# Kernel optimization log

Measured on AMD Instinct MI355X. Metric: run time of the kernel, lower is better.

Reference implementation:

```python
import jax, jax.numpy as jnp
import numpy as np

EMB = 1024
HEADS = 16


def setup_inputs() -> dict:
    key = jax.random.key(0)
    ks = jax.random.split(key, 5)
    s = 1.0 / np.sqrt(EMB).astype(np.float32)
    return {
        "x": jax.random.normal(ks[0], (4, 2048, EMB), dtype=jnp.float32),
        "Wq": jax.random.normal(ks[1], (EMB, EMB), dtype=jnp.float32) * s,
        "bq": jnp.zeros((EMB,), dtype=jnp.float32),
        "Wk": jax.random.normal(ks[2], (EMB, EMB), dtype=jnp.float32) * s,
        "bk": jnp.zeros((EMB,), dtype=jnp.float32),
        "Wv": jax.random.normal(ks[3], (EMB, EMB), dtype=jnp.float32) * s,
        "bv": jnp.zeros((EMB,), dtype=jnp.float32),
        "Wo": jax.random.normal(ks[4], (EMB, EMB), dtype=jnp.float32) * s,
        "bo": jnp.zeros((EMB,), dtype=jnp.float32),
    }


def reference(x, Wq, bq, Wk, bk, Wv, bv, Wo, bo):
    b, n, e = x.shape
    h = HEADS
    d = e // h
    # QKV projections, split heads: [b, n, e] -> [b, h, n, d]
    def split_heads(t):
        return t.reshape(b, n, h, d).transpose(0, 2, 1, 3)
    q = split_heads(x @ Wq + bq)
    k = split_heads(x @ Wk + bk)
    v = split_heads(x @ Wv + bv)
    # NOTE: original scales by sqrt(emb_size), not sqrt(head_dim)
    energy = jnp.einsum('bhqd,bhkd->bhqk', q, k)
    att = jax.nn.softmax(energy / jnp.sqrt(jnp.float32(e)), axis=-1)
    # dropout is identity in eval mode
    out = jnp.einsum('bhqk,bhkd->bhqd', att, v)
    out = out.transpose(0, 2, 1, 3).reshape(b, n, e)
    return out @ Wo + bo
```

## Files before the change

### kernel.cpp

```cpp
#include <hip/hip_runtime.h>

#define EMB   1024
#define SEQ   2048
#define BATCH 4
#define HEADS 16
#define HDIM  64
#define MTOT  8192

typedef __bf16 bf16x8 __attribute__((ext_vector_type(8)));
typedef float  fx4    __attribute__((ext_vector_type(4)));

#if __has_builtin(__builtin_amdgcn_exp2f)
#define EXP2(x) __builtin_amdgcn_exp2f(x)
#else
#define EXP2(x) exp2f(x)
#endif

__device__ __forceinline__ unsigned short f2bf(float f) {
    unsigned u = __builtin_bit_cast(unsigned, f);
    u += 0x7fffu + ((u >> 16) & 1u);
    return (unsigned short)(u >> 16);
}
__device__ __forceinline__ unsigned short bfbits(float f) {
    __bf16 h = (__bf16)f;
    return __builtin_bit_cast(unsigned short, h);
}

#define AS1 __attribute__((address_space(1)))
#define AS3 __attribute__((address_space(3)))
__device__ __forceinline__ void glds16(const void* g, void* l) {
    __builtin_amdgcn_global_load_lds((AS1 void*)g, (AS3 void*)l, 16, 0, 0);
}
#define DRAIN_GLDS() __builtin_amdgcn_s_waitcnt(0x0f70)

#define QSCALE 0.0450842137604569f

__global__ __launch_bounds__(256) void cvt_x_kernel(const float* __restrict__ x,
                                                    unsigned short* __restrict__ xb)
{
    const int idx = (blockIdx.x * 256 + threadIdx.x) * 4;
    const float4 v = *(const float4*)(x + idx);
    ushort4 o;
    o.x = f2bf(v.x); o.y = f2bf(v.y); o.z = f2bf(v.z); o.w = f2bf(v.w);
    *(ushort4*)(xb + idx) = o;
}

__global__ __launch_bounds__(256) void cvt_w_kernel(
    const float* __restrict__ w0, const float* __restrict__ w1,
    const float* __restrict__ w2, const float* __restrict__ w3,
    unsigned short* __restrict__ o0, unsigned short* __restrict__ o1,
    unsigned short* __restrict__ o2, unsigned short* __restrict__ o3)
{
    const int z = blockIdx.z;
    const float* W = z == 0 ? w0 : (z == 1 ? w1 : (z == 2 ? w2 : w3));
    unsigned short* O = z == 0 ? o0 : (z == 1 ? o1 : (z == 2 ? o2 : o3));

    __shared__ float Ws[64][65];
    const int t  = threadIdx.x;
    const int k0 = blockIdx.x * 64, n0 = blockIdx.y * 64;
#pragma unroll
    for (int p = 0; p < 4; ++p) {
        const int row = p * 16 + (t >> 4);
        const int col = (t & 15) * 4;
        const float4 v = *(const float4*)(W + (size_t)(k0 + row) * EMB + n0 + col);
        Ws[row][col]     = v.x; Ws[row][col + 1] = v.y;
        Ws[row][col + 2] = v.z; Ws[row][col + 3] = v.w;
    }
    __syncthreads();
    const int nn = t >> 2;
    const int kb = (t & 3) * 16;
#pragma unroll
    for (int q = 0; q < 2; ++q) {
        const int kk = kb + q * 8;
        ushort4 u0, u1;
        u0.x = f2bf(Ws[kk + 0][nn]); u0.y = f2bf(Ws[kk + 1][nn]);
        u0.z = f2bf(Ws[kk + 2][nn]); u0.w = f2bf(Ws[kk + 3][nn]);
        u1.x = f2bf(Ws[kk + 4][nn]); u1.y = f2bf(Ws[kk + 5][nn]);
        u1.z = f2bf(Ws[kk + 6][nn]); u1.w = f2bf(Ws[kk + 7][nn]);
        *(ushort4*)(O + (size_t)(n0 + nn) * EMB + k0 + kk)     = u0;
        *(ushort4*)(O + (size_t)(n0 + nn) * EMB + k0 + kk + 4) = u1;
    }
}

__global__ __launch_bounds__(256) void gemm_bf16_kernel(
    const unsigned short* __restrict__ Ag,
    const unsigned short* __restrict__ B0, const unsigned short* __restrict__ B1,
    const unsigned short* __restrict__ B2,
    const float* __restrict__ bias0, const float* __restrict__ bias1,
    const float* __restrict__ bias2,
    void* out0, void* out1, void* out2, int mode)
{
    const int z = blockIdx.z;
    const unsigned short* __restrict__ Bg = z == 0 ? B0 : (z == 1 ? B1 : B2);
    const float* __restrict__ bias = z == 0 ? bias0 : (z == 1 ? bias1 : bias2);
    void* outp = z == 0 ? out0 : (z == 1 ? out1 : out2);

    __shared__ unsigned short As[128][32];
    __shared__ unsigned short Bs[128][32];

    const int t    = threadIdx.x;
    const int w    = t >> 6;
    const int lane = t & 63;
    const int low4 = lane & 15;
    const int quad = lane >> 4;
    const int m0 = blockIdx.x * 128;
    const int e0 = blockIdx.y * 128;
    const int we = (w & 1) * 64;
    const int wm = (w >> 1) * 64;

    const int srow   = w * 32 + (lane >> 2);
    const int schunk = (lane & 3) ^ ((lane >> 3) & 3);
    const int scol   = schunk * 8;

    const int fchunk = (quad ^ ((low4 >> 1) & 3)) * 8;

    fx4 acc[4][4] = {};

    for (int k0 = 0; k0 < EMB; k0 += 32) {
        __syncthreads();
        glds16(Ag + (size_t)(m0 + srow) * EMB + k0 + scol,      &As[w * 32][0]);
        glds16(Ag + (size_t)(m0 + srow + 16) * EMB + k0 + scol, &As[w * 32 + 16][0]);
        glds16(Bg + (size_t)(e0 + srow) * EMB + k0 + scol,      &Bs[w * 32][0]);
        glds16(Bg + (size_t)(e0 + srow + 16) * EMB + k0 + scol, &Bs[w * 32 + 16][0]);
        DRAIN_GLDS();
        __syncthreads();

        bf16x8 af[4], bfr[4];
#pragma unroll
        for (int i = 0; i < 4; ++i) {
            af[i]  = *(const bf16x8*)&Bs[we + i * 16 + low4][fchunk];
            bfr[i] = *(const bf16x8*)&As[wm + i * 16 + low4][fchunk];
        }
#pragma unroll
        for (int i = 0; i < 4; ++i)
#pragma unroll
            for (int j = 0; j < 4; ++j)
                acc[i][j] = __builtin_amdgcn_mfma_f32_16x16x32_bf16(af[i], bfr[j], acc[i][j], 0, 0, 0);
    }

    fx4 bv[4];
#pragma unroll
    for (int i = 0; i < 4; ++i)
        bv[i] = *(const fx4*)(bias + e0 + we + i * 16 + quad * 4);

    if (mode == 1) {
#pragma unroll
        for (int i = 0; i < 4; ++i)
#pragma unroll
            for (int j = 0; j < 4; ++j) {
                const int m  = m0 + wm + j * 16 + low4;
                const int eb = e0 + we + i * 16 + quad * 4;
                fx4 o4;
#pragma unroll
                for (int rr = 0; rr < 4; ++rr) o4[rr] = acc[i][j][rr] + bv[i][rr];
                *(fx4*)((float*)outp + (size_t)m * EMB + eb) = o4;
            }
    } else if (z <= 1) {
        const float sc = (z == 0) ? QSCALE : 1.0f;
        unsigned short* o = (unsigned short*)outp;
#pragma unroll
        for (int i = 0; i < 4; ++i)
#pragma unroll
            for (int j = 0; j < 4; ++j) {
                const int m  = m0 + wm + j * 16 + low4;
                const int eb = e0 + we + i * 16 + quad * 4;
                const int bb = m >> 11, n = m & (SEQ - 1);
                const int hh = eb >> 6, db = eb & 63;
                ushort4 o4;
                o4.x = f2bf((acc[i][j][0] + bv[i][0]) * sc);
                o4.y = f2bf((acc[i][j][1] + bv[i][1]) * sc);
                o4.z = f2bf((acc[i][j][2] + bv[i][2]) * sc);
                o4.w = f2bf((acc[i][j][3] + bv[i][3]) * sc);
                *(ushort4*)(o + (((size_t)(bb * HEADS + hh)) * SEQ + n) * HDIM + db) = o4;
            }
    } else {
        unsigned short* o = (unsigned short*)outp;
        const int mbase = m0 + wm;
        const int bb    = mbase >> 11;
        const int nb    = mbase & (SEQ - 1);
#pragma unroll
        for (int i = 0; i < 4; ++i) {
            const int eb = e0 + we + i * 16 + quad * 4;
            const int hh = eb >> 6, db = eb & 63;
#pragma unroll
            for (int rr = 0; rr < 4; ++rr) {
                ushort4 o4;
                o4.x = f2bf(acc[i][0][rr] + bv[i][rr]);
                o4.y = f2bf(acc[i][1][rr] + bv[i][rr]);
                o4.z = f2bf(acc[i][2][rr] + bv[i][rr]);
                o4.w = f2bf(acc[i][3][rr] + bv[i][rr]);
                *(ushort4*)(o + (((size_t)(bb * HEADS + hh)) * HDIM + db + rr) * SEQ
                              + nb + low4 * 4) = o4;
            }
        }
    }
}

__global__ __launch_bounds__(256, 2) void attn_mfma4_kernel(
    const unsigned short* __restrict__ qg, const unsigned short* __restrict__ kg,
    const unsigned short* __restrict__ vg, unsigned short* __restrict__ attb)
{
    __shared__ unsigned short Ks[2][64][64];
    __shared__ unsigned short Vs[2][64][64];
    __shared__ unsigned short Ps[4][4][16][72];

    const int t    = threadIdx.x;
    const int w    = t >> 6;
    const int lane = t & 63;
    const int low4 = lane & 15;
    const int quad = lane >> 4;
    const int q0   = blockIdx.x * 256 + w * 64;
    const int bh   = blockIdx.y;
    const size_t base = (size_t)bh * SEQ * HDIM;

    const int srow8  = lane >> 3;
    const int schunk = (lane & 7) ^ srow8;

    bf16x8 aq[4][2];
#pragma unroll
    for (int s = 0; s < 4; ++s) {
        const size_t qrow = base + (size_t)(q0 + s * 16 + low4) * HDIM;
        aq[s][0] = *(const bf16x8*)(qg + qrow + quad * 8);
        aq[s][1] = *(const bf16x8*)(qg + qrow + 32 + quad * 8);
    }

    fx4 o_acc[4][4] = {};
    float l_i[4][4] = {};
    const fx4 fzero = {0.f, 0.f, 0.f, 0.f};

    {
        const unsigned short* kp = kg + base + (size_t)(w * 16 + srow8) * HDIM + schunk * 8;
        glds16(kp,              &Ks[0][w * 16][0]);
        glds16(kp + 8 * HDIM,   &Ks[0][w * 16 + 8][0]);
        const unsigned short* vp = vg + base + (size_t)(w * 16 + srow8) * SEQ + schunk * 8;
        glds16(vp,              &Vs[0][w * 16][0]);
        glds16(vp + 8 * SEQ,    &Vs[0][w * 16 + 8][0]);
    }

    for (int tt0 = 0; tt0 < SEQ / 64; ++tt0) {
        const int buf = tt0 & 1;
        DRAIN_GLDS();
        __syncthreads();

        bf16x8 kf[4][2], vf[4][2];
#pragma unroll
        for (int tk = 0; tk < 4; ++tk) {
            const int row = tk * 16 + low4;
            const int x7  = low4 & 7;
#pragma unroll
            for (int c = 0; c < 2; ++c) {
                const int lc = (c * 4 + quad) ^ x7;
                kf[tk][c] = *(const bf16x8*)&Ks[buf][row][lc * 8];
                vf[tk][c] = *(const bf16x8*)&Vs[buf][row][lc * 8];
            }
        }

        if (tt0 + 1 < SEQ / 64) {
            const int kv1 = (tt0 + 1) * 64;
            const unsigned short* kp = kg + base + (size_t)(kv1 + w * 16 + srow8) * HDIM + schunk * 8;
            glds16(kp,            &Ks[buf ^ 1][w * 16][0]);
            glds16(kp + 8 * HDIM, &Ks[buf ^ 1][w * 16 + 8][0]);
            const unsigned short* vp = vg + base + (size_t)(w * 16 + srow8) * SEQ + kv1 + schunk * 8;
            glds16(vp,            &Vs[buf ^ 1][w * 16][0]);
            glds16(vp + 8 * SEQ,  &Vs[buf ^ 1][w * 16 + 8][0]);
        }

#pragma unroll
        for (int s = 0; s < 4; ++s) {
            fx4 sa[4];
#pragma unroll
            for (int tk = 0; tk < 4; ++tk) {
                sa[tk] = __builtin_amdgcn_mfma_f32_16x16x32_bf16(aq[s][0], kf[tk][0], fzero, 0, 0, 0);
                sa[tk] = __builtin_amdgcn_mfma_f32_16x16x32_bf16(aq[s][1], kf[tk][1], sa[tk], 0, 0, 0);
            }
#pragma unroll
            for (int r = 0; r < 4; ++r) {
                const float p0 = EXP2(sa[0][r]);
                const float p1 = EXP2(sa[1][r]);
                const float p2 = EXP2(sa[2][r]);
                const float p3 = EXP2(sa[3][r]);
                l_i[s][r] += (p0 + p1) + (p2 + p3);
                uint2 pk;
                pk.x = (unsigned)bfbits(p0) | ((unsigned)bfbits(p1) << 16);
                pk.y = (unsigned)bfbits(p2) | ((unsigned)bfbits(p3) << 16);
                *(uint2*)&Ps[w][s][quad * 4 + r][low4 * 4] = pk;
            }
            bf16x8 pf0 = *(const bf16x8*)&Ps[w][s][low4][quad * 8];
            bf16x8 pf1 = *(const bf16x8*)&Ps[w][s][low4][32 + quad * 8];
#pragma unroll
            for (int t2 = 0; t2 < 4; ++t2) {
                o_acc[s][t2] = __builtin_amdgcn_mfma_f32_16x16x32_bf16(pf0, vf[t2][0], o_acc[s][t2], 0, 0, 0);
                o_acc[s][t2] = __builtin_amdgcn_mfma_f32_16x16x32_bf16(pf1, vf[t2][1], o_acc[s][t2], 0, 0, 0);
            }
        }
    }

#pragma unroll
    for (int s = 0; s < 4; ++s)
#pragma unroll
        for (int r = 0; r < 4; ++r) {
            float v = l_i[s][r];
            for (int off = 1; off < 16; off <<= 1)
                v += __shfl_xor(v, off, 16);
            l_i[s][r] = 1.0f / v;
        }

    const int bb = bh >> 4, hh = bh & 15;
#pragma unroll
    for (int s = 0; s < 4; ++s)
#pragma unroll
        for (int r = 0; r < 4; ++r) {
            const size_t m = (size_t)bb * SEQ + q0 + s * 16 + quad * 4 + r;
#pragma unroll
            for (int t2 = 0; t2 < 4; ++t2) {
                const int e = hh * HDIM + t2 * 16 + low4;
                attb[m * EMB + e] = bfbits(o_acc[s][t2][r] * l_i[s][r]);
            }
        }
}

extern "C" void kernel_launch(void* const* d_in, const int* in_sizes, int n_in,
                              void* d_out, int out_size, void* d_ws, size_t ws_size,
                              hipStream_t stream)
{
    const float* x  = (const float*)d_in[0];
    const float* Wq = (const float*)d_in[1];
    const float* bq = (const float*)d_in[2];
    const float* Wk = (const float*)d_in[3];
    const float* bk = (const float*)d_in[4];
    const float* Wv = (const float*)d_in[5];
    const float* bv = (const float*)d_in[6];
    const float* Wo = (const float*)d_in[7];
    const float* bo = (const float*)d_in[8];

    unsigned short* ws  = (unsigned short*)d_ws;
    unsigned short* xb  = ws;
    unsigned short* wqt = xb + 8388608;
    unsigned short* wkt = wqt + 1048576;
    unsigned short* wvt = wkt + 1048576;
    unsigned short* wot = wvt + 1048576;
    unsigned short* qb  = wot + 1048576;
    unsigned short* kbuf = qb + 8388608;
    unsigned short* vtb  = kbuf + 8388608;
    unsigned short* attb = vtb + 8388608;

    cvt_x_kernel<<<8192, 256, 0, stream>>>(x, xb);
    cvt_w_kernel<<<dim3(16, 16, 4), 256, 0, stream>>>(Wq, Wk, Wv, Wo, wqt, wkt, wvt, wot);

    gemm_bf16_kernel<<<dim3(64, 8, 3), 256, 0, stream>>>(
        xb, wqt, wkt, wvt, bq, bk, bv, qb, kbuf, vtb, 0);

    attn_mfma4_kernel<<<dim3(8, 64), 256, 0, stream>>>(qb, kbuf, vtb, attb);

    gemm_bf16_kernel<<<dim3(64, 8, 1), 256, 0, stream>>>(
        attb, wot, wot, wot, bo, bo, bo, d_out, d_out, d_out, 1);
}
```

Baseline: 284.0 us.

## Deepen GEMM K-tile to 64 and restructure attention K staging and LDS

The GEMM now stages 64-wide K slices per barrier pair with an XOR swizzle over eight chunks, which halves the number of synchronisations and global-to-LDS drains per output tile. The attention kernel stops staging K in shared memory and reads K fragments straight from global memory. It also shrinks the P scratch buffer to one slot per wave and raises the occupancy hint to 3 blocks per CU. The grid is flattened so consecutive blocks cover different heads. The trade-offs are uncoalesced or cache-dependent direct K loads, and reuse of a single P buffer that depends on a compiler barrier for correct ordering.

```diff
diff --git a/kernel.cpp b/kernel.cpp
--- a/kernel.cpp
+++ b/kernel.cpp
@@ -95,8 +95,8 @@
     const float* __restrict__ bias = z == 0 ? bias0 : (z == 1 ? bias1 : bias2);
     void* outp = z == 0 ? out0 : (z == 1 ? out1 : out2);
 
-    __shared__ unsigned short As[128][32];
-    __shared__ unsigned short Bs[128][32];
+    __shared__ unsigned short As[128][64];
+    __shared__ unsigned short Bs[128][64];
 
     const int t    = threadIdx.x;
     const int w    = t >> 6;
@@ -108,34 +108,38 @@
     const int we = (w & 1) * 64;
     const int wm = (w >> 1) * 64;
 
-    const int srow   = w * 32 + (lane >> 2);
-    const int schunk = (lane & 3) ^ ((lane >> 3) & 3);
-    const int scol   = schunk * 8;
-
-    const int fchunk = (quad ^ ((low4 >> 1) & 3)) * 8;
+    const int srow8 = lane >> 3;
+    const int scg   = ((lane & 7) ^ srow8) * 8;
+    const int x7    = low4 & 7;
 
     fx4 acc[4][4] = {};
 
-    for (int k0 = 0; k0 < EMB; k0 += 32) {
+    for (int k0 = 0; k0 < EMB; k0 += 64) {
         __syncthreads();
-        glds16(Ag + (size_t)(m0 + srow) * EMB + k0 + scol,      &As[w * 32][0]);
-        glds16(Ag + (size_t)(m0 + srow + 16) * EMB + k0 + scol, &As[w * 32 + 16][0]);
-        glds16(Bg + (size_t)(e0 + srow) * EMB + k0 + scol,      &Bs[w * 32][0]);
-        glds16(Bg + (size_t)(e0 + srow + 16) * EMB + k0 + scol, &Bs[w * 32 + 16][0]);
+#pragma unroll
+        for (int g = 0; g < 4; ++g) {
+            const int r = w * 32 + g * 8;
+            glds16(Ag + (size_t)(m0 + r + srow8) * EMB + k0 + scg, &As[r][0]);
+            glds16(Bg + (size_t)(e0 + r + srow8) * EMB + k0 + scg, &Bs[r][0]);
+        }
         DRAIN_GLDS();
         __syncthreads();
 
-        bf16x8 af[4], bfr[4];
-#pragma unroll
-        for (int i = 0; i < 4; ++i) {
-            af[i]  = *(const bf16x8*)&Bs[we + i * 16 + low4][fchunk];
-            bfr[i] = *(const bf16x8*)&As[wm + i * 16 + low4][fchunk];
-        }
-#pragma unroll
-        for (int i = 0; i < 4; ++i)
-#pragma unroll
-            for (int j = 0; j < 4; ++j)
-                acc[i][j] = __builtin_amdgcn_mfma_f32_16x16x32_bf16(af[i], bfr[j], acc[i][j], 0, 0, 0);
+#pragma unroll
+        for (int h = 0; h < 2; ++h) {
+            const int fc = ((h * 4 + quad) ^ x7) * 8;
+            bf16x8 af[4], bfr[4];
+#pragma unroll
+            for (int i = 0; i < 4; ++i) {
+                af[i]  = *(const bf16x8*)&Bs[we + i * 16 + low4][fc];
+                bfr[i] = *(const bf16x8*)&As[wm + i * 16 + low4][fc];
+            }
+#pragma unroll
+            for (int i = 0; i < 4; ++i)
+#pragma unroll
+                for (int j = 0; j < 4; ++j)
+                    acc[i][j] = __builtin_amdgcn_mfma_f32_16x16x32_bf16(af[i], bfr[j], acc[i][j], 0, 0, 0);
+        }
     }
 
     fx4 bv[4];
@@ -196,25 +200,27 @@
     }
 }
 
-__global__ __launch_bounds__(256, 2) void attn_mfma4_kernel(
+__global__ __launch_bounds__(256, 3) void attn_mfma5_kernel(
     const unsigned short* __restrict__ qg, const unsigned short* __restrict__ kg,
     const unsigned short* __restrict__ vg, unsigned short* __restrict__ attb)
 {
-    __shared__ unsigned short Ks[2][64][64];
     __shared__ unsigned short Vs[2][64][64];
-    __shared__ unsigned short Ps[4][4][16][72];
+    __shared__ unsigned short Ps[4][16][72];
 
     const int t    = threadIdx.x;
     const int w    = t >> 6;
     const int lane = t & 63;
     const int low4 = lane & 15;
     const int quad = lane >> 4;
-    const int q0   = blockIdx.x * 256 + w * 64;
-    const int bh   = blockIdx.y;
+    const int id   = blockIdx.x;
+    const int bh   = id & 63;
+    const int qblk = id >> 6;
+    const int q0   = qblk * 256 + w * 64;
     const size_t base = (size_t)bh * SEQ * HDIM;
 
     const int srow8  = lane >> 3;
     const int schunk = (lane & 7) ^ srow8;
+    const int x7     = low4 & 7;
 
     bf16x8 aq[4][2];
 #pragma unroll
@@ -229,40 +235,41 @@
     const fx4 fzero = {0.f, 0.f, 0.f, 0.f};
 
     {
-        const unsigned short* kp = kg + base + (size_t)(w * 16 + srow8) * HDIM + schunk * 8;
-        glds16(kp,              &Ks[0][w * 16][0]);
-        glds16(kp + 8 * HDIM,   &Ks[0][w * 16 + 8][0]);
         const unsigned short* vp = vg + base + (size_t)(w * 16 + srow8) * SEQ + schunk * 8;
-        glds16(vp,              &Vs[0][w * 16][0]);
-        glds16(vp + 8 * SEQ,    &Vs[0][w * 16 + 8][0]);
+        glds16(vp,           &Vs[0][w * 16][0]);
+        glds16(vp + 8 * SEQ, &Vs[0][w * 16 + 8][0]);
     }
 
     for (int tt0 = 0; tt0 < SEQ / 64; ++tt0) {
         const int buf = tt0 & 1;
+        const int kv0 = tt0 * 64;
         DRAIN_GLDS();
         __syncthreads();
 
-        bf16x8 kf[4][2], vf[4][2];
+        bf16x8 kf[4][2];
 #pragma unroll
         for (int tk = 0; tk < 4; ++tk) {
-            const int row = tk * 16 + low4;
-            const int x7  = low4 & 7;
+            const size_t krow = base + (size_t)(kv0 + tk * 16 + low4) * HDIM;
+            kf[tk][0] = *(const bf16x8*)(kg + krow + quad * 8);
+            kf[tk][1] = *(const bf16x8*)(kg + krow + 32 + quad * 8);
+        }
+
+        bf16x8 vf[4][2];
+#pragma unroll
+        for (int t2 = 0; t2 < 4; ++t2) {
+            const int row = t2 * 16 + low4;
 #pragma unroll
             for (int c = 0; c < 2; ++c) {
                 const int lc = (c * 4 + quad) ^ x7;
-                kf[tk][c] = *(const bf16x8*)&Ks[buf][row][lc * 8];
-                vf[tk][c] = *(const bf16x8*)&Vs[buf][row][lc * 8];
+                vf[t2][c] = *(const bf16x8*)&Vs[buf][row][lc * 8];
             }
         }
 
         if (tt0 + 1 < SEQ / 64) {
-            const int kv1 = (tt0 + 1) * 64;
-            const unsigned short* kp = kg + base + (size_t)(kv1 + w * 16 + srow8) * HDIM + schunk * 8;
-            glds16(kp,            &Ks[buf ^ 1][w * 16][0]);
-            glds16(kp + 8 * HDIM, &Ks[buf ^ 1][w * 16 + 8][0]);
-            const unsigned short* vp = vg + base + (size_t)(w * 16 + srow8) * SEQ + kv1 + schunk * 8;
-            glds16(vp,            &Vs[buf ^ 1][w * 16][0]);
-            glds16(vp + 8 * SEQ,  &Vs[buf ^ 1][w * 16 + 8][0]);
+            const unsigned short* vp = vg + base + (size_t)(w * 16 + srow8) * SEQ
+                                     + (kv0 + 64) + schunk * 8;
+            glds16(vp,           &Vs[buf ^ 1][w * 16][0]);
+            glds16(vp + 8 * SEQ, &Vs[buf ^ 1][w * 16 + 8][0]);
         }
 
 #pragma unroll
@@ -283,10 +290,11 @@
                 uint2 pk;
                 pk.x = (unsigned)bfbits(p0) | ((unsigned)bfbits(p1) << 16);
                 pk.y = (unsigned)bfbits(p2) | ((unsigned)bfbits(p3) << 16);
-                *(uint2*)&Ps[w][s][quad * 4 + r][low4 * 4] = pk;
-            }
-            bf16x8 pf0 = *(const bf16x8*)&Ps[w][s][low4][quad * 8];
-            bf16x8 pf1 = *(const bf16x8*)&Ps[w][s][low4][32 + quad * 8];
+                *(uint2*)&Ps[w][quad * 4 + r][low4 * 4] = pk;
+            }
+            __asm__ volatile("" ::: "memory");
+            bf16x8 pf0 = *(const bf16x8*)&Ps[w][low4][quad * 8];
+            bf16x8 pf1 = *(const bf16x8*)&Ps[w][low4][32 + quad * 8];
 #pragma unroll
             for (int t2 = 0; t2 < 4; ++t2) {
                 o_acc[s][t2] = __builtin_amdgcn_mfma_f32_16x16x32_bf16(pf0, vf[t2][0], o_acc[s][t2], 0, 0, 0);
@@ -350,7 +358,7 @@
     gemm_bf16_kernel<<<dim3(64, 8, 3), 256, 0, stream>>>(
         xb, wqt, wkt, wvt, bq, bk, bv, qb, kbuf, vtb, 0);
 
-    attn_mfma4_kernel<<<dim3(8, 64), 256, 0, stream>>>(qb, kbuf, vtb, attb);
+    attn_mfma5_kernel<<<512, 256, 0, stream>>>(qb, kbuf, vtb, attb);
 
     gemm_bf16_kernel<<<dim3(64, 8, 1), 256, 0, stream>>>(
         attb, wot, wot, wot, bo, bo, bo, d_out, d_out, d_out, 1);
```

Result: slower. 412.7 us (+45.3%).
